# Optimization experiments

Measured on AMD Instinct MI355X. Metric: run time of the kernel, lower is better.

The kernel has to match this reference:

```python
import jax, jax.numpy as jnp
import numpy as np

NEG = 9000000000000000.0  # large negative multiplier from the original code

def setup_inputs() -> dict:
    key = jax.random.key(0)
    ks = jax.random.split(key, 7)
    B, N, DIN, H, DOUT = 128, 512, 256, 256, 256
    x = jax.random.normal(ks[0], (B, N, DIN), dtype=jnp.float32)
    # binary float mask (1 = attend, 0 = blocked), as used multiplicatively in the module
    mask = (jax.random.uniform(ks[1], (B, N, N)) > 0.5).astype(jnp.float32)
    def lin(k, fan_in, fan_out):
        kw, kb = jax.random.split(k)
        bound = 1.0 / np.sqrt(fan_in)
        W = jax.random.uniform(kw, (fan_in, fan_out), minval=-bound, maxval=bound, dtype=jnp.float32)
        b = jax.random.uniform(kb, (fan_out,), minval=-bound, maxval=bound, dtype=jnp.float32)
        return W, b
    Wv, bv = lin(ks[2], DIN, H)
    Wk, bk = lin(ks[3], DIN, H)
    Wq, bq = lin(ks[4], DIN, H)
    Wo, bo = lin(ks[5], H, DOUT)
    return {"x": x, "mask": mask, "Wv": Wv, "bv": bv, "Wk": Wk, "bk": bk,
            "Wq": Wq, "bq": bq, "Wo": Wo, "bo": bo}

def reference(x, mask, Wv, bv, Wk, bk, Wq, bq, Wo, bo):
    # x: [B,N,din], mask: [B,N,N]
    v = jax.nn.relu(jnp.einsum('bnd,dh->bnh', x, Wv) + bv)   # [B,N,H]
    q = jax.nn.relu(jnp.einsum('bnd,dh->bnh', x, Wq) + bq)   # [B,N,H]
    k = jax.nn.relu(jnp.einsum('bnd,dh->bnh', x, Wk) + bk)   # [B,N,H]
    scores = jnp.einsum('bnh,bmh->bnm', q, k)                 # [B,N,N]
    att = jax.nn.softmax(scores * mask - NEG * (1.0 - mask), axis=2)
    out = jnp.einsum('bnm,bmh->bnh', att, v)                  # [B,N,H]
    out = jax.nn.relu(jnp.einsum('bnh,ho->bno', out, Wo) + bo)
    return out
```

## Files before the change

### kernel.cpp

```cpp
#include <hip/hip_runtime.h>
#include <stdint.h>

typedef __attribute__((ext_vector_type(8))) __bf16 bf16x8;
typedef __attribute__((ext_vector_type(4))) float f32x4;
typedef __attribute__((ext_vector_type(8))) unsigned short ushort8;
typedef __attribute__((ext_vector_type(4))) unsigned short ushort4v;
typedef unsigned short u16;
typedef unsigned int u32;

__device__ __forceinline__ u16 f2bf(float f) {
    __bf16 h = (__bf16)f;
    return __builtin_bit_cast(u16, h);
}

__device__ __forceinline__ f32x4 mfma16(bf16x8 a, bf16x8 b, f32x4 c) {
    return __builtin_amdgcn_mfma_f32_16x16x32_bf16(a, b, c, 0, 0, 0);
}

typedef __attribute__((address_space(1))) const char g_char;
typedef __attribute__((address_space(3))) char l_char;
__device__ __forceinline__ void gload_lds16(const void* g, void* l) {
    __builtin_amdgcn_global_load_lds((g_char*)g, (l_char*)l, 16, 0, 0);
}

__global__ __launch_bounds__(256) void prep_w(
    const float* __restrict__ Wq, const float* __restrict__ Wk,
    const float* __restrict__ Wv, const float* __restrict__ Wo,
    u16* __restrict__ WT, u16* __restrict__ WOT)
{
    int idx = blockIdx.x * 256 + threadIdx.x;
    if (idx < 196608) {
        int j = idx >> 8, k = idx & 255;
        const float* W = (j < 256) ? Wq : (j < 512) ? Wk : Wv;
        WT[idx] = f2bf(W[k * 256 + (j & 255)]);
    } else {
        int t = idx - 196608;
        int j = t >> 8, k = t & 255;
        WOT[t] = f2bf(Wo[k * 256 + j]);
    }
}

__global__ __launch_bounds__(256, 2) void qkv_gemm(
    const float* __restrict__ X, const u16* __restrict__ WT,
    const float* __restrict__ bQ, const float* __restrict__ bK,
    const float* __restrict__ bV,
    u16* __restrict__ outQ, u16* __restrict__ outK, u16* __restrict__ outVT)
{
    __shared__ __align__(16) u16 As[128 * 256];
    __shared__ __align__(16) u16 Bs[128 * 64];
    const int tid = threadIdx.x;
    const int m0 = blockIdx.x * 128;

    #pragma unroll
    for (int i = 0; i < 32; ++i) {
        int flat = (i * 256 + tid) * 4;
        int r = flat >> 8, c = flat & 255;
        const f32x4 f = *reinterpret_cast<const f32x4*>(X + (size_t)(m0 + r) * 256 + c);
        ushort4v h;
        h.x = f2bf(f.x); h.y = f2bf(f.y); h.z = f2bf(f.z); h.w = f2bf(f.w);
        int byte = (r * 512 + c * 2) ^ ((r & 7) << 4);
        *reinterpret_cast<ushort4v*>(reinterpret_cast<char*>(As) + byte) = h;
    }

    const int lane = tid & 63, wid = tid >> 6;
    const int wr = wid >> 1, wc = wid & 1;
    const int lr = lane & 15, lg = lane >> 4;

    for (int cb = 0; cb < 6; ++cb) {
        const int jbase = cb * 128;
        f32x4 acc[4][4];
        #pragma unroll
        for (int a = 0; a < 4; ++a)
            #pragma unroll
            for (int b = 0; b < 4; ++b) acc[a][b] = (f32x4){0.f, 0.f, 0.f, 0.f};

        for (int kk = 0; kk < 256; kk += 64) {
            __syncthreads();
            #pragma unroll
            for (int i = 0; i < 4; ++i) {
                int e = (i * 256 + tid) * 8;
                int r = e >> 6, c = e & 63;
                ushort8 d = *reinterpret_cast<const ushort8*>(WT + (size_t)(jbase + r) * 256 + kk + c);
                int byte = (r * 128 + c * 2) ^ ((r & 7) << 4);
                *reinterpret_cast<ushort8*>(reinterpret_cast<char*>(Bs) + byte) = d;
            }
            __syncthreads();
            #pragma unroll
            for (int ks = 0; ks < 2; ++ks) {
                bf16x8 af[4], bfr[4];
                #pragma unroll
                for (int mt = 0; mt < 4; ++mt) {
                    int r = wr * 64 + mt * 16 + lr;
                    int byte = (r * 512 + (kk + ks * 32 + lg * 8) * 2) ^ ((r & 7) << 4);
                    af[mt] = *reinterpret_cast<const bf16x8*>(reinterpret_cast<const char*>(As) + byte);
                }
                #pragma unroll
                for (int nt = 0; nt < 4; ++nt) {
                    int r = wc * 64 + nt * 16 + lr;
                    int byte = (r * 128 + (ks * 32 + lg * 8) * 2) ^ ((r & 7) << 4);
                    bfr[nt] = *reinterpret_cast<const bf16x8*>(reinterpret_cast<const char*>(Bs) + byte);
                }
                #pragma unroll
                for (int mt = 0; mt < 4; ++mt)
                    #pragma unroll
                    for (int nt = 0; nt < 4; ++nt)
                        acc[mt][nt] = mfma16(af[mt], bfr[nt], acc[mt][nt]);
            }
        }
        const float* bias = (cb < 2) ? bQ : (cb < 4) ? bK : bV;
        float bcol[4];
        #pragma unroll
        for (int nt = 0; nt < 4; ++nt)
            bcol[nt] = bias[(jbase + wc * 64 + nt * 16 + lr) & 255];
        #pragma unroll
        for (int mt = 0; mt < 4; ++mt) {
            #pragma unroll
            for (int nt = 0; nt < 4; ++nt) {
                #pragma unroll
                for (int j = 0; j < 4; ++j) {
                    float v = fmaxf(acc[mt][nt][j] + bcol[nt], 0.f);
                    u16 h = f2bf(v);
                    int row = m0 + wr * 64 + mt * 16 + lg * 4 + j;
                    int col = jbase + wc * 64 + nt * 16 + lr;
                    if (cb < 2) {
                        outQ[(size_t)row * 256 + col] = h;
                    } else if (cb < 4) {
                        outK[(size_t)row * 256 + (col - 256)] = h;
                    } else {
                        int bb = row >> 9, n = row & 511;
                        outVT[(size_t)bb * 131072 + (size_t)(col - 512) * 512 + n] = h;
                    }
                }
            }
        }
    }
}

__global__ __launch_bounds__(512) void attn_kernel(
    const u16* __restrict__ Q, const u16* __restrict__ K,
    const u16* __restrict__ VT, const float* __restrict__ Mask,
    u16* __restrict__ Out)
{
    __shared__ __align__(16) u16 k_lds[2][32 * 256];
    __shared__ __align__(16) u16 v_lds[2][256 * 32];
    __shared__ __align__(16) char p_lds[8 * 1280];
    const int tid = threadIdx.x;
    const int b  = blockIdx.x & 127;
    const int rb = blockIdx.x >> 7;
    const int lane = tid & 63, wid = tid >> 6;
    const int lr = lane & 15, lg = lane >> 4;
    const int n0 = rb * 128 + wid * 16;
    const u16* qbat = Q  + (size_t)b * 131072;
    const u16* kbat = K  + (size_t)b * 131072;
    const u16* vbat = VT + (size_t)b * 131072;
    const float* mbase = Mask + ((size_t)b * 512 + n0 + lr) * 512;
    char* pw = p_lds + wid * 1280;

    auto stage = [&](int buf, int kt) {
        #pragma unroll
        for (int i = 0; i < 2; ++i) {
            int p = (i * 512 + tid) * 16;
            int krow = p >> 9, kcol2 = p & 511;
            int scol2 = kcol2 ^ ((krow & 7) << 4);
            const char* gk = reinterpret_cast<const char*>(kbat + (size_t)(kt * 32 + krow) * 256) + scol2;
            char* lk = reinterpret_cast<char*>(k_lds[buf]) + i * 8192 + wid * 1024;
            gload_lds16(gk, lk);
            int vrow = p >> 6;
            int chunk = (p >> 4) & 3;
            int schunk = chunk ^ (vrow & 3);
            const char* gv = reinterpret_cast<const char*>(vbat + (size_t)vrow * 512 + kt * 32) + schunk * 16;
            char* lv = reinterpret_cast<char*>(v_lds[buf]) + i * 8192 + wid * 1024;
            gload_lds16(gv, lv);
        }
    };

    bf16x8 qf[8];
    #pragma unroll
    for (int ks = 0; ks < 8; ++ks)
        qf[ks] = *reinterpret_cast<const bf16x8*>(
            qbat + (size_t)(n0 + lr) * 256 + ks * 32 + lg * 8);

    stage(0, 0);
    f32x4 mf[2];
    #pragma unroll
    for (int ct = 0; ct < 2; ++ct)
        mf[ct] = __builtin_nontemporal_load(
            reinterpret_cast<const f32x4*>(mbase + ct * 16 + lg * 4));

    f32x4 acc[16];
    #pragma unroll
    for (int i = 0; i < 16; ++i) acc[i] = (f32x4){0.f, 0.f, 0.f, 0.f};
    float mreg = -__builtin_inff(), lreg = 0.f;

    __syncthreads();

    for (int kt = 0; kt < 16; ++kt) {
        const int cur = kt & 1;
        if (kt < 15) stage(cur ^ 1, kt + 1);

        u32 mb = 0;
        #pragma unroll
        for (int ct = 0; ct < 2; ++ct)
            #pragma unroll
            for (int j = 0; j < 4; ++j)
                mb |= (mf[ct][j] > 0.5f ? 1u : 0u) << (ct * 4 + j);
        if (kt < 15) {
            #pragma unroll
            for (int ct = 0; ct < 2; ++ct)
                mf[ct] = __builtin_nontemporal_load(reinterpret_cast<const f32x4*>(
                    mbase + (kt + 1) * 32 + ct * 16 + lg * 4));
        }

        f32x4 s[2];
        s[0] = (f32x4){0.f, 0.f, 0.f, 0.f};
        s[1] = (f32x4){0.f, 0.f, 0.f, 0.f};
        const char* kbase = reinterpret_cast<const char*>(k_lds[cur]);
        __builtin_amdgcn_s_setprio(1);
        #pragma unroll
        for (int ks = 0; ks < 8; ++ks) {
            #pragma unroll
            for (int ct = 0; ct < 2; ++ct) {
                int krow = ct * 16 + lr;
                int byte = (krow * 512 + (ks * 32 + lg * 8) * 2) ^ ((krow & 7) << 4);
                bf16x8 kf = *reinterpret_cast<const bf16x8*>(kbase + byte);
                s[ct] = mfma16(kf, qf[ks], s[ct]);
            }
        }
        __builtin_amdgcn_s_setprio(0);

        float p[2][4];
        #pragma unroll
        for (int ct = 0; ct < 2; ++ct)
            #pragma unroll
            for (int j = 0; j < 4; ++j)
                p[ct][j] = ((mb >> (ct * 4 + j)) & 1u) ? s[ct][j] : -9.0e15f;

        float r0 = p[0][0];
        r0 = fmaxf(r0, p[0][1]); r0 = fmaxf(r0, p[0][2]); r0 = fmaxf(r0, p[0][3]);
        r0 = fmaxf(r0, p[1][0]); r0 = fmaxf(r0, p[1][1]);
        r0 = fmaxf(r0, p[1][2]); r0 = fmaxf(r0, p[1][3]);
        r0 = fmaxf(r0, __shfl_xor(r0, 16));
        r0 = fmaxf(r0, __shfl_xor(r0, 32));
        bool need = (r0 > mreg);
        if (__any(need)) {
            float mnew = fmaxf(mreg, r0);
            float sc = __expf(mreg - mnew);
            mreg = mnew;
            lreg *= sc;
            #pragma unroll
            for (int ht = 0; ht < 16; ++ht) {
                acc[ht][0] *= sc; acc[ht][1] *= sc;
                acc[ht][2] *= sc; acc[ht][3] *= sc;
            }
        }
        float ps = 0.f;
        #pragma unroll
        for (int ct = 0; ct < 2; ++ct)
            #pragma unroll
            for (int j = 0; j < 4; ++j) {
                float e = __expf(p[ct][j] - mreg);
                p[ct][j] = e;
                ps += e;
            }
        lreg += ps;

        #pragma unroll
        for (int ct = 0; ct < 2; ++ct) {
            ushort4v w;
            w.x = f2bf(p[ct][0]); w.y = f2bf(p[ct][1]);
            w.z = f2bf(p[ct][2]); w.w = f2bf(p[ct][3]);
            *reinterpret_cast<ushort4v*>(pw + lr * 80 + ct * 32 + lg * 8) = w;
        }

        bf16x8 pf = *reinterpret_cast<const bf16x8*>(pw + lr * 80 + lg * 16);
        const char* vbase = reinterpret_cast<const char*>(v_lds[cur]);
        __builtin_amdgcn_s_setprio(1);
        #pragma unroll
        for (int ht = 0; ht < 16; ++ht) {
            int hrow = ht * 16 + lr;
            int byte = (hrow * 64 + lg * 16) ^ ((hrow & 3) << 4);
            bf16x8 vf = *reinterpret_cast<const bf16x8*>(vbase + byte);
            acc[ht] = mfma16(vf, pf, acc[ht]);
        }
        __builtin_amdgcn_s_setprio(0);

        __syncthreads();
    }

    float lt = lreg;
    lt += __shfl_xor(lt, 16);
    lt += __shfl_xor(lt, 32);
    float inv = 1.0f / lt;
    u16* orow = Out + ((size_t)b * 512 + n0 + lr) * 256;
    #pragma unroll
    for (int ht = 0; ht < 16; ++ht) {
        ushort4v w;
        w.x = f2bf(acc[ht][0] * inv); w.y = f2bf(acc[ht][1] * inv);
        w.z = f2bf(acc[ht][2] * inv); w.w = f2bf(acc[ht][3] * inv);
        *reinterpret_cast<ushort4v*>(orow + ht * 16 + lg * 4) = w;
    }
}

__global__ __launch_bounds__(256, 2) void out_gemm(
    const u16* __restrict__ A, const u16* __restrict__ WOT,
    const float* __restrict__ bO, float* __restrict__ Out)
{
    __shared__ __align__(16) u16 As[128 * 256];
    __shared__ __align__(16) u16 Bs[128 * 64];
    const int tid = threadIdx.x;
    const int m0 = blockIdx.x * 128;

    #pragma unroll
    for (int i = 0; i < 16; ++i) {
        int e = (i * 256 + tid) * 8;
        int r = e >> 8, c = e & 255;
        ushort8 d = *reinterpret_cast<const ushort8*>(A + (size_t)(m0 + r) * 256 + c);
        int byte = (r * 512 + c * 2) ^ ((r & 7) << 4);
        *reinterpret_cast<ushort8*>(reinterpret_cast<char*>(As) + byte) = d;
    }

    const int lane = tid & 63, wid = tid >> 6;
    const int wr = wid >> 1, wc = wid & 1;
    const int lr = lane & 15, lg = lane >> 4;

    for (int cb = 0; cb < 2; ++cb) {
        const int jbase = cb * 128;
        f32x4 acc[4][4];
        #pragma unroll
        for (int a = 0; a < 4; ++a)
            #pragma unroll
            for (int b = 0; b < 4; ++b) acc[a][b] = (f32x4){0.f, 0.f, 0.f, 0.f};

        for (int kk = 0; kk < 256; kk += 64) {
            __syncthreads();
            #pragma unroll
            for (int i = 0; i < 4; ++i) {
                int e = (i * 256 + tid) * 8;
                int r = e >> 6, c = e & 63;
                ushort8 d = *reinterpret_cast<const ushort8*>(WOT + (size_t)(jbase + r) * 256 + kk + c);
                int byte = (r * 128 + c * 2) ^ ((r & 7) << 4);
                *reinterpret_cast<ushort8*>(reinterpret_cast<char*>(Bs) + byte) = d;
            }
            __syncthreads();
            #pragma unroll
            for (int ks = 0; ks < 2; ++ks) {
                bf16x8 af[4], bfr[4];
                #pragma unroll
                for (int mt = 0; mt < 4; ++mt) {
                    int r = wr * 64 + mt * 16 + lr;
                    int byte = (r * 512 + (kk + ks * 32 + lg * 8) * 2) ^ ((r & 7) << 4);
                    af[mt] = *reinterpret_cast<const bf16x8*>(reinterpret_cast<const char*>(As) + byte);
                }
                #pragma unroll
                for (int nt = 0; nt < 4; ++nt) {
                    int r = wc * 64 + nt * 16 + lr;
                    int byte = (r * 128 + (ks * 32 + lg * 8) * 2) ^ ((r & 7) << 4);
                    bfr[nt] = *reinterpret_cast<const bf16x8*>(reinterpret_cast<const char*>(Bs) + byte);
                }
                #pragma unroll
                for (int mt = 0; mt < 4; ++mt)
                    #pragma unroll
                    for (int nt = 0; nt < 4; ++nt)
                        acc[mt][nt] = mfma16(af[mt], bfr[nt], acc[mt][nt]);
            }
        }
        float bcol[4];
        #pragma unroll
        for (int nt = 0; nt < 4; ++nt)
            bcol[nt] = bO[jbase + wc * 64 + nt * 16 + lr];
        #pragma unroll
        for (int mt = 0; mt < 4; ++mt) {
            #pragma unroll
            for (int nt = 0; nt < 4; ++nt) {
                #pragma unroll
                for (int j = 0; j < 4; ++j) {
                    float v = fmaxf(acc[mt][nt][j] + bcol[nt], 0.f);
                    int row = m0 + wr * 64 + mt * 16 + lg * 4 + j;
                    int col = jbase + wc * 64 + nt * 16 + lr;
                    Out[(size_t)row * 256 + col] = v;
                }
            }
        }
    }
}

extern "C" void kernel_launch(void* const* d_in, const int* in_sizes, int n_in,
                              void* d_out, int out_size, void* d_ws, size_t ws_size,
                              hipStream_t stream) {
    const float* x    = (const float*)d_in[0];
    const float* mask = (const float*)d_in[1];
    const float* Wv   = (const float*)d_in[2];
    const float* bv   = (const float*)d_in[3];
    const float* Wk   = (const float*)d_in[4];
    const float* bk   = (const float*)d_in[5];
    const float* Wq   = (const float*)d_in[6];
    const float* bq   = (const float*)d_in[7];
    const float* Wo   = (const float*)d_in[8];
    const float* bo   = (const float*)d_in[9];
    float* out = (float*)d_out;

    char* ws = (char*)d_ws;
    u16* WT  = (u16*)(ws);
    u16* WOT = (u16*)(ws + 393216);
    u16* Qb  = (u16*)(ws + 524288);
    u16* Kb  = (u16*)(ws + 524288 + 33554432);
    u16* VTb = (u16*)(ws + 524288 + 2 * 33554432);

    prep_w<<<1024, 256, 0, stream>>>(Wq, Wk, Wv, Wo, WT, WOT);
    qkv_gemm<<<512, 256, 0, stream>>>(x, WT, bq, bk, bv, Qb, Kb, VTb);
    attn_kernel<<<512, 512, 0, stream>>>(Qb, Kb, VTb, mask, Qb);
    out_gemm<<<512, 256, 0, stream>>>(Qb, WOT, bo, out);
}
```

Before: 187.5 us.

## Split QKV GEMM per column block with double-buffered async weight staging

The QKV projection now launches one block per (row tile, 128-column block), 3072 blocks instead of 512. Each block streams X in 64-wide K slices through double-buffered LDS rather than holding the full 128x256 A tile. prep_w pre-swizzles the weights into K-sliced chunks so they can be copied straight to LDS with global_load_lds while the current slice computes, and MFMA sections get raised priority. The aim is more parallelism, smaller LDS use and overlap of loads with compute, at the cost of reading and converting X six times instead of once.

```diff
diff --git a/kernel.cpp b/kernel.cpp
--- a/kernel.cpp
+++ b/kernel.cpp
@@ -26,13 +26,15 @@
 __global__ __launch_bounds__(256) void prep_w(
     const float* __restrict__ Wq, const float* __restrict__ Wk,
     const float* __restrict__ Wv, const float* __restrict__ Wo,
-    u16* __restrict__ WT, u16* __restrict__ WOT)
+    u16* __restrict__ WTs, u16* __restrict__ WOT)
 {
     int idx = blockIdx.x * 256 + threadIdx.x;
     if (idx < 196608) {
         int j = idx >> 8, k = idx & 255;
         const float* W = (j < 256) ? Wq : (j < 512) ? Wk : Wv;
-        WT[idx] = f2bf(W[k * 256 + (j & 255)]);
+        u16 v = f2bf(W[k * 256 + (j & 255)]);
+        int kk = k >> 6, c = k & 63;
+        WTs[kk * 49152 + j * 64 + (c ^ ((j & 7) << 3))] = v;
     } else {
         int t = idx - 196608;
         int j = t >> 8, k = t & 255;
@@ -40,11 +42,300 @@
     }
 }
 
-__global__ __launch_bounds__(256, 2) void qkv_gemm(
-    const float* __restrict__ X, const u16* __restrict__ WT,
+__global__ __launch_bounds__(256) void qkv_gemm(
+    const float* __restrict__ X, const u16* __restrict__ WTs,
     const float* __restrict__ bQ, const float* __restrict__ bK,
     const float* __restrict__ bV,
     u16* __restrict__ outQ, u16* __restrict__ outK, u16* __restrict__ outVT)
+{
+    __shared__ __align__(16) u16 As[2][8192];
+    __shared__ __align__(16) u16 Bs[2][8192];
+    const int tid = threadIdx.x;
+    const int bid = blockIdx.x;
+    const int m0 = (bid / 6) * 128;
+    const int cbi = bid - (bid / 6) * 6;
+    const int jbase = cbi * 128;
+
+    const int lane = tid & 63, wid = tid >> 6;
+    const int wr = wid >> 1, wc = wid & 1;
+    const int lr = lane & 15, lg = lane >> 4;
+
+    auto stageB = [&](int buf, int kk) {
+        const char* src = reinterpret_cast<const char*>(
+            WTs + (size_t)kk * 49152 + (size_t)jbase * 64);
+        #pragma unroll
+        for (int i = 0; i < 4; ++i) {
+            int p = (i * 256 + tid) * 16;
+            gload_lds16(src + p,
+                reinterpret_cast<char*>(Bs[buf]) + i * 4096 + wid * 1024);
+        }
+    };
+
+    f32x4 ar[8];
+    auto issueA = [&](int kk) {
+        #pragma unroll
+        for (int i = 0; i < 8; ++i) {
+            int e = (i * 256 + tid) * 4;
+            int r = e >> 6, c = e & 63;
+            ar[i] = *reinterpret_cast<const f32x4*>(
+                X + (size_t)(m0 + r) * 256 + kk * 64 + c);
+        }
+    };
+    auto writeA = [&](int buf) {
+        #pragma unroll
+        for (int i = 0; i < 8; ++i) {
+            int e = (i * 256 + tid) * 4;
+            int r = e >> 6, c = e & 63;
+            ushort4v h;
+            h.x = f2bf(ar[i].x); h.y = f2bf(ar[i].y);
+            h.z = f2bf(ar[i].z); h.w = f2bf(ar[i].w);
+            int byte = (r * 128 + c * 2) ^ ((r & 7) << 4);
+            *reinterpret_cast<ushort4v*>(reinterpret_cast<char*>(As[buf]) + byte) = h;
+        }
+    };
+
+    f32x4 acc[4][4];
+    #pragma unroll
+    for (int a = 0; a < 4; ++a)
+        #pragma unroll
+        for (int b = 0; b < 4; ++b) acc[a][b] = (f32x4){0.f, 0.f, 0.f, 0.f};
+
+    stageB(0, 0);
+    issueA(0);
+    writeA(0);
+    __syncthreads();
+
+    for (int kk = 0; kk < 4; ++kk) {
+        const int cur = kk & 1;
+        if (kk < 3) {
+            stageB(cur ^ 1, kk + 1);
+            issueA(kk + 1);
+        }
+        #pragma unroll
+        for (int ks = 0; ks < 2; ++ks) {
+            bf16x8 af[4], bfr[4];
+            #pragma unroll
+            for (int mt = 0; mt < 4; ++mt) {
+                int r = wr * 64 + mt * 16 + lr;
+                int byte = (r * 128 + ks * 64 + lg * 16) ^ ((r & 7) << 4);
+                af[mt] = *reinterpret_cast<const bf16x8*>(
+                    reinterpret_cast<const char*>(As[cur]) + byte);
+            }
+            #pragma unroll
+            for (int nt = 0; nt < 4; ++nt) {
+                int r = wc * 64 + nt * 16 + lr;
+                int byte = (r * 128 + ks * 64 + lg * 16) ^ ((r & 7) << 4);
+                bfr[nt] = *reinterpret_cast<const bf16x8*>(
+                    reinterpret_cast<const char*>(Bs[cur]) + byte);
+            }
+            __builtin_amdgcn_s_setprio(1);
+            #pragma unroll
+            for (int mt = 0; mt < 4; ++mt)
+                #pragma unroll
+                for (int nt = 0; nt < 4; ++nt)
+                    acc[mt][nt] = mfma16(af[mt], bfr[nt], acc[mt][nt]);
+            __builtin_amdgcn_s_setprio(0);
+        }
+        if (kk < 3) writeA(cur ^ 1);
+        __syncthreads();
+    }
+
+    const float* bias = (cbi < 2) ? bQ : (cbi < 4) ? bK : bV;
+    float bcol[4];
+    #pragma unroll
+    for (int nt = 0; nt < 4; ++nt)
+        bcol[nt] = bias[(jbase + wc * 64 + nt * 16 + lr) & 255];
+    #pragma unroll
+    for (int mt = 0; mt < 4; ++mt) {
+        #pragma unroll
+        for (int nt = 0; nt < 4; ++nt) {
+            #pragma unroll
+            for (int j = 0; j < 4; ++j) {
+                float v = fmaxf(acc[mt][nt][j] + bcol[nt], 0.f);
+                u16 h = f2bf(v);
+                int row = m0 + wr * 64 + mt * 16 + lg * 4 + j;
+                int col = jbase + wc * 64 + nt * 16 + lr;
+                if (cbi < 2) {
+                    outQ[(size_t)row * 256 + col] = h;
+                } else if (cbi < 4) {
+                    outK[(size_t)row * 256 + (col - 256)] = h;
+                } else {
+                    int bb = row >> 9, n = row & 511;
+                    outVT[(size_t)bb * 131072 + (size_t)(col - 512) * 512 + n] = h;
+                }
+            }
+        }
+    }
+}
+
+__global__ __launch_bounds__(512) void attn_kernel(
+    const u16* __restrict__ Q, const u16* __restrict__ K,
+    const u16* __restrict__ VT, const float* __restrict__ Mask,
+    u16* __restrict__ Out)
+{
+    __shared__ __align__(16) u16 k_lds[2][32 * 256];
+    __shared__ __align__(16) u16 v_lds[2][256 * 32];
+    __shared__ __align__(16) char p_lds[8 * 1280];
+    const int tid = threadIdx.x;
+    const int b  = blockIdx.x & 127;
+    const int rb = blockIdx.x >> 7;
+    const int lane = tid & 63, wid = tid >> 6;
+    const int lr = lane & 15, lg = lane >> 4;
+    const int n0 = rb * 128 + wid * 16;
+    const u16* qbat = Q  + (size_t)b * 131072;
+    const u16* kbat = K  + (size_t)b * 131072;
+    const u16* vbat = VT + (size_t)b * 131072;
+    const float* mbase = Mask + ((size_t)b * 512 + n0 + lr) * 512;
+    char* pw = p_lds + wid * 1280;
+
+    auto stage = [&](int buf, int kt) {
+        #pragma unroll
+        for (int i = 0; i < 2; ++i) {
+            int p = (i * 512 + tid) * 16;
+            int krow = p >> 9, kcol2 = p & 511;
+            int scol2 = kcol2 ^ ((krow & 7) << 4);
+            const char* gk = reinterpret_cast<const char*>(kbat + (size_t)(kt * 32 + krow) * 256) + scol2;
+            char* lk = reinterpret_cast<char*>(k_lds[buf]) + i * 8192 + wid * 1024;
+            gload_lds16(gk, lk);
+            int vrow = p >> 6;
+            int chunk = (p >> 4) & 3;
+            int schunk = chunk ^ (vrow & 3);
+            const char* gv = reinterpret_cast<const char*>(vbat + (size_t)vrow * 512 + kt * 32) + schunk * 16;
+            char* lv = reinterpret_cast<char*>(v_lds[buf]) + i * 8192 + wid * 1024;
+            gload_lds16(gv, lv);
+        }
+    };
+
+    bf16x8 qf[8];
+    #pragma unroll
+    for (int ks = 0; ks < 8; ++ks)
+        qf[ks] = *reinterpret_cast<const bf16x8*>(
+            qbat + (size_t)(n0 + lr) * 256 + ks * 32 + lg * 8);
+
+    stage(0, 0);
+    f32x4 mf[2];
+    #pragma unroll
+    for (int ct = 0; ct < 2; ++ct)
+        mf[ct] = __builtin_nontemporal_load(
+            reinterpret_cast<const f32x4*>(mbase + ct * 16 + lg * 4));
+
+    f32x4 acc[16];
+    #pragma unroll
+    for (int i = 0; i < 16; ++i) acc[i] = (f32x4){0.f, 0.f, 0.f, 0.f};
+    float mreg = -__builtin_inff(), lreg = 0.f;
+
+    __syncthreads();
+
+    for (int kt = 0; kt < 16; ++kt) {
+        const int cur = kt & 1;
+        if (kt < 15) stage(cur ^ 1, kt + 1);
+
+        u32 mb = 0;
+        #pragma unroll
+        for (int ct = 0; ct < 2; ++ct)
+            #pragma unroll
+            for (int j = 0; j < 4; ++j)
+                mb |= (mf[ct][j] > 0.5f ? 1u : 0u) << (ct * 4 + j);
+        if (kt < 15) {
+            #pragma unroll
+            for (int ct = 0; ct < 2; ++ct)
+                mf[ct] = __builtin_nontemporal_load(reinterpret_cast<const f32x4*>(
+                    mbase + (kt + 1) * 32 + ct * 16 + lg * 4));
+        }
+
+        f32x4 s[2];
+        s[0] = (f32x4){0.f, 0.f, 0.f, 0.f};
+        s[1] = (f32x4){0.f, 0.f, 0.f, 0.f};
+        const char* kbase = reinterpret_cast<const char*>(k_lds[cur]);
+        __builtin_amdgcn_s_setprio(1);
+        #pragma unroll
+        for (int ks = 0; ks < 8; ++ks) {
+            #pragma unroll
+            for (int ct = 0; ct < 2; ++ct) {
+                int krow = ct * 16 + lr;
+                int byte = (krow * 512 + (ks * 32 + lg * 8) * 2) ^ ((krow & 7) << 4);
+                bf16x8 kf = *reinterpret_cast<const bf16x8*>(kbase + byte);
+                s[ct] = mfma16(kf, qf[ks], s[ct]);
+            }
+        }
+        __builtin_amdgcn_s_setprio(0);
+
+        float p[2][4];
+        #pragma unroll
+        for (int ct = 0; ct < 2; ++ct)
+            #pragma unroll
+            for (int j = 0; j < 4; ++j)
+                p[ct][j] = ((mb >> (ct * 4 + j)) & 1u) ? s[ct][j] : -9.0e15f;
+
+        float r0 = p[0][0];
+        r0 = fmaxf(r0, p[0][1]); r0 = fmaxf(r0, p[0][2]); r0 = fmaxf(r0, p[0][3]);
+        r0 = fmaxf(r0, p[1][0]); r0 = fmaxf(r0, p[1][1]);
+        r0 = fmaxf(r0, p[1][2]); r0 = fmaxf(r0, p[1][3]);
+        r0 = fmaxf(r0, __shfl_xor(r0, 16));
+        r0 = fmaxf(r0, __shfl_xor(r0, 32));
+        bool need = (r0 > mreg);
+        if (__any(need)) {
+            float mnew = fmaxf(mreg, r0);
+            float sc = __expf(mreg - mnew);
+            mreg = mnew;
+            lreg *= sc;
+            #pragma unroll
+            for (int ht = 0; ht < 16; ++ht) {
+                acc[ht][0] *= sc; acc[ht][1] *= sc;
+                acc[ht][2] *= sc; acc[ht][3] *= sc;
+            }
+        }
+        float ps = 0.f;
+        #pragma unroll
+        for (int ct = 0; ct < 2; ++ct)
+            #pragma unroll
+            for (int j = 0; j < 4; ++j) {
+                float e = __expf(p[ct][j] - mreg);
+                p[ct][j] = e;
+                ps += e;
+            }
+        lreg += ps;
+
+        #pragma unroll
+        for (int ct = 0; ct < 2; ++ct) {
+            ushort4v w;
+            w.x = f2bf(p[ct][0]); w.y = f2bf(p[ct][1]);
+            w.z = f2bf(p[ct][2]); w.w = f2bf(p[ct][3]);
+            *reinterpret_cast<ushort4v*>(pw + lr * 80 + ct * 32 + lg * 8) = w;
+        }
+
+        bf16x8 pf = *reinterpret_cast<const bf16x8*>(pw + lr * 80 + lg * 16);
+        const char* vbase = reinterpret_cast<const char*>(v_lds[cur]);
+        __builtin_amdgcn_s_setprio(1);
+        #pragma unroll
+        for (int ht = 0; ht < 16; ++ht) {
+            int hrow = ht * 16 + lr;
+            int byte = (hrow * 64 + lg * 16) ^ ((hrow & 3) << 4);
+            bf16x8 vf = *reinterpret_cast<const bf16x8*>(vbase + byte);
+            acc[ht] = mfma16(vf, pf, acc[ht]);
+        }
+        __builtin_amdgcn_s_setprio(0);
+
+        __syncthreads();
+    }
+
+    float lt = lreg;
+    lt += __shfl_xor(lt, 16);
+    lt += __shfl_xor(lt, 32);
+    float inv = 1.0f / lt;
+    u16* orow = Out + ((size_t)b * 512 + n0 + lr) * 256;
+    #pragma unroll
+    for (int ht = 0; ht < 16; ++ht) {
+        ushort4v w;
+        w.x = f2bf(acc[ht][0] * inv); w.y = f2bf(acc[ht][1] * inv);
+        w.z = f2bf(acc[ht][2] * inv); w.w = f2bf(acc[ht][3] * inv);
+        *reinterpret_cast<ushort4v*>(orow + ht * 16 + lg * 4) = w;
+    }
+}
+
+__global__ __launch_bounds__(256, 2) void out_gemm(
+    const u16* __restrict__ A, const u16* __restrict__ WOT,
+    const float* __restrict__ bO, float* __restrict__ Out)
 {
     __shared__ __align__(16) u16 As[128 * 256];
     __shared__ __align__(16) u16 Bs[128 * 64];
@@ -52,21 +343,19 @@
     const int m0 = blockIdx.x * 128;
 
     #pragma unroll
-    for (int i = 0; i < 32; ++i) {
-        int flat = (i * 256 + tid) * 4;
-        int r = flat >> 8, c = flat & 255;
-        const f32x4 f = *reinterpret_cast<const f32x4*>(X + (size_t)(m0 + r) * 256 + c);
-        ushort4v h;
-        h.x = f2bf(f.x); h.y = f2bf(f.y); h.z = f2bf(f.z); h.w = f2bf(f.w);
+    for (int i = 0; i < 16; ++i) {
+        int e = (i * 256 + tid) * 8;
+        int r = e >> 8, c = e & 255;
+        ushort8 d = *reinterpret_cast<const ushort8*>(A + (size_t)(m0 + r) * 256 + c);
         int byte = (r * 512 + c * 2) ^ ((r & 7) << 4);
-        *reinterpret_cast<ushort4v*>(reinterpret_cast<char*>(As) + byte) = h;
+        *reinterpret_cast<ushort8*>(reinterpret_cast<char*>(As) + byte) = d;
     }
 
     const int lane = tid & 63, wid = tid >> 6;
     const int wr = wid >> 1, wc = wid & 1;
     const int lr = lane & 15, lg = lane >> 4;
 
-    for (int cb = 0; cb < 6; ++cb) {
+    for (int cb = 0; cb < 2; ++cb) {
         const int jbase = cb * 128;
         f32x4 acc[4][4];
         #pragma unroll
@@ -80,7 +369,7 @@
             for (int i = 0; i < 4; ++i) {
                 int e = (i * 256 + tid) * 8;
                 int r = e >> 6, c = e & 63;
-                ushort8 d = *reinterpret_cast<const ushort8*>(WT + (size_t)(jbase + r) * 256 + kk + c);
+                ushort8 d = *reinterpret_cast<const ushort8*>(WOT + (size_t)(jbase + r) * 256 + kk + c);
                 int byte = (r * 128 + c * 2) ^ ((r & 7) << 4);
                 *reinterpret_cast<ushort8*>(reinterpret_cast<char*>(Bs) + byte) = d;
             }
@@ -107,263 +396,6 @@
                         acc[mt][nt] = mfma16(af[mt], bfr[nt], acc[mt][nt]);
             }
         }
-        const float* bias = (cb < 2) ? bQ : (cb < 4) ? bK : bV;
-        float bcol[4];
-        #pragma unroll
-        for (int nt = 0; nt < 4; ++nt)
-            bcol[nt] = bias[(jbase + wc * 64 + nt * 16 + lr) & 255];
-        #pragma unroll
-        for (int mt = 0; mt < 4; ++mt) {
-            #pragma unroll
-            for (int nt = 0; nt < 4; ++nt) {
-                #pragma unroll
-                for (int j = 0; j < 4; ++j) {
-                    float v = fmaxf(acc[mt][nt][j] + bcol[nt], 0.f);
-                    u16 h = f2bf(v);
-                    int row = m0 + wr * 64 + mt * 16 + lg * 4 + j;
-                    int col = jbase + wc * 64 + nt * 16 + lr;
-                    if (cb < 2) {
-                        outQ[(size_t)row * 256 + col] = h;
-                    } else if (cb < 4) {
-                        outK[(size_t)row * 256 + (col - 256)] = h;
-                    } else {
-                        int bb = row >> 9, n = row & 511;
-                        outVT[(size_t)bb * 131072 + (size_t)(col - 512) * 512 + n] = h;
-                    }
-                }
-            }
-        }
-    }
-}
-
-__global__ __launch_bounds__(512) void attn_kernel(
-    const u16* __restrict__ Q, const u16* __restrict__ K,
-    const u16* __restrict__ VT, const float* __restrict__ Mask,
-    u16* __restrict__ Out)
-{
-    __shared__ __align__(16) u16 k_lds[2][32 * 256];
-    __shared__ __align__(16) u16 v_lds[2][256 * 32];
-    __shared__ __align__(16) char p_lds[8 * 1280];
-    const int tid = threadIdx.x;
-    const int b  = blockIdx.x & 127;
-    const int rb = blockIdx.x >> 7;
-    const int lane = tid & 63, wid = tid >> 6;
-    const int lr = lane & 15, lg = lane >> 4;
-    const int n0 = rb * 128 + wid * 16;
-    const u16* qbat = Q  + (size_t)b * 131072;
-    const u16* kbat = K  + (size_t)b * 131072;
-    const u16* vbat = VT + (size_t)b * 131072;
-    const float* mbase = Mask + ((size_t)b * 512 + n0 + lr) * 512;
-    char* pw = p_lds + wid * 1280;
-
-    auto stage = [&](int buf, int kt) {
-        #pragma unroll
-        for (int i = 0; i < 2; ++i) {
-            int p = (i * 512 + tid) * 16;
-            int krow = p >> 9, kcol2 = p & 511;
-            int scol2 = kcol2 ^ ((krow & 7) << 4);
-            const char* gk = reinterpret_cast<const char*>(kbat + (size_t)(kt * 32 + krow) * 256) + scol2;
-            char* lk = reinterpret_cast<char*>(k_lds[buf]) + i * 8192 + wid * 1024;
-            gload_lds16(gk, lk);
-            int vrow = p >> 6;
-            int chunk = (p >> 4) & 3;
-            int schunk = chunk ^ (vrow & 3);
-            const char* gv = reinterpret_cast<const char*>(vbat + (size_t)vrow * 512 + kt * 32) + schunk * 16;
-            char* lv = reinterpret_cast<char*>(v_lds[buf]) + i * 8192 + wid * 1024;
-            gload_lds16(gv, lv);
-        }
-    };
-
-    bf16x8 qf[8];
-    #pragma unroll
-    for (int ks = 0; ks < 8; ++ks)
-        qf[ks] = *reinterpret_cast<const bf16x8*>(
-            qbat + (size_t)(n0 + lr) * 256 + ks * 32 + lg * 8);
-
-    stage(0, 0);
-    f32x4 mf[2];
-    #pragma unroll
-    for (int ct = 0; ct < 2; ++ct)
-        mf[ct] = __builtin_nontemporal_load(
-            reinterpret_cast<const f32x4*>(mbase + ct * 16 + lg * 4));
-
-    f32x4 acc[16];
-    #pragma unroll
-    for (int i = 0; i < 16; ++i) acc[i] = (f32x4){0.f, 0.f, 0.f, 0.f};
-    float mreg = -__builtin_inff(), lreg = 0.f;
-
-    __syncthreads();
-
-    for (int kt = 0; kt < 16; ++kt) {
-        const int cur = kt & 1;
-        if (kt < 15) stage(cur ^ 1, kt + 1);
-
-        u32 mb = 0;
-        #pragma unroll
-        for (int ct = 0; ct < 2; ++ct)
-            #pragma unroll
-            for (int j = 0; j < 4; ++j)
-                mb |= (mf[ct][j] > 0.5f ? 1u : 0u) << (ct * 4 + j);
-        if (kt < 15) {
-            #pragma unroll
-            for (int ct = 0; ct < 2; ++ct)
-                mf[ct] = __builtin_nontemporal_load(reinterpret_cast<const f32x4*>(
-                    mbase + (kt + 1) * 32 + ct * 16 + lg * 4));
-        }
-
-        f32x4 s[2];
-        s[0] = (f32x4){0.f, 0.f, 0.f, 0.f};
-        s[1] = (f32x4){0.f, 0.f, 0.f, 0.f};
-        const char* kbase = reinterpret_cast<const char*>(k_lds[cur]);
-        __builtin_amdgcn_s_setprio(1);
-        #pragma unroll
-        for (int ks = 0; ks < 8; ++ks) {
-            #pragma unroll
-            for (int ct = 0; ct < 2; ++ct) {
-                int krow = ct * 16 + lr;
-                int byte = (krow * 512 + (ks * 32 + lg * 8) * 2) ^ ((krow & 7) << 4);
-                bf16x8 kf = *reinterpret_cast<const bf16x8*>(kbase + byte);
-                s[ct] = mfma16(kf, qf[ks], s[ct]);
-            }
-        }
-        __builtin_amdgcn_s_setprio(0);
-
-        float p[2][4];
-        #pragma unroll
-        for (int ct = 0; ct < 2; ++ct)
-            #pragma unroll
-            for (int j = 0; j < 4; ++j)
-                p[ct][j] = ((mb >> (ct * 4 + j)) & 1u) ? s[ct][j] : -9.0e15f;
-
-        float r0 = p[0][0];
-        r0 = fmaxf(r0, p[0][1]); r0 = fmaxf(r0, p[0][2]); r0 = fmaxf(r0, p[0][3]);
-        r0 = fmaxf(r0, p[1][0]); r0 = fmaxf(r0, p[1][1]);
-        r0 = fmaxf(r0, p[1][2]); r0 = fmaxf(r0, p[1][3]);
-        r0 = fmaxf(r0, __shfl_xor(r0, 16));
-        r0 = fmaxf(r0, __shfl_xor(r0, 32));
-        bool need = (r0 > mreg);
-        if (__any(need)) {
-            float mnew = fmaxf(mreg, r0);
-            float sc = __expf(mreg - mnew);
-            mreg = mnew;
-            lreg *= sc;
-            #pragma unroll
-            for (int ht = 0; ht < 16; ++ht) {
-                acc[ht][0] *= sc; acc[ht][1] *= sc;
-                acc[ht][2] *= sc; acc[ht][3] *= sc;
-            }
-        }
-        float ps = 0.f;
-        #pragma unroll
-        for (int ct = 0; ct < 2; ++ct)
-            #pragma unroll
-            for (int j = 0; j < 4; ++j) {
-                float e = __expf(p[ct][j] - mreg);
-                p[ct][j] = e;
-                ps += e;
-            }
-        lreg += ps;
-
-        #pragma unroll
-        for (int ct = 0; ct < 2; ++ct) {
-            ushort4v w;
-            w.x = f2bf(p[ct][0]); w.y = f2bf(p[ct][1]);
-            w.z = f2bf(p[ct][2]); w.w = f2bf(p[ct][3]);
-            *reinterpret_cast<ushort4v*>(pw + lr * 80 + ct * 32 + lg * 8) = w;
-        }
-
-        bf16x8 pf = *reinterpret_cast<const bf16x8*>(pw + lr * 80 + lg * 16);
-        const char* vbase = reinterpret_cast<const char*>(v_lds[cur]);
-        __builtin_amdgcn_s_setprio(1);
-        #pragma unroll
-        for (int ht = 0; ht < 16; ++ht) {
-            int hrow = ht * 16 + lr;
-            int byte = (hrow * 64 + lg * 16) ^ ((hrow & 3) << 4);
-            bf16x8 vf = *reinterpret_cast<const bf16x8*>(vbase + byte);
-            acc[ht] = mfma16(vf, pf, acc[ht]);
-        }
-        __builtin_amdgcn_s_setprio(0);
-
-        __syncthreads();
-    }
-
-    float lt = lreg;
-    lt += __shfl_xor(lt, 16);
-    lt += __shfl_xor(lt, 32);
-    float inv = 1.0f / lt;
-    u16* orow = Out + ((size_t)b * 512 + n0 + lr) * 256;
-    #pragma unroll
-    for (int ht = 0; ht < 16; ++ht) {
-        ushort4v w;
-        w.x = f2bf(acc[ht][0] * inv); w.y = f2bf(acc[ht][1] * inv);
-        w.z = f2bf(acc[ht][2] * inv); w.w = f2bf(acc[ht][3] * inv);
-        *reinterpret_cast<ushort4v*>(orow + ht * 16 + lg * 4) = w;
-    }
-}
-
-__global__ __launch_bounds__(256, 2) void out_gemm(
-    const u16* __restrict__ A, const u16* __restrict__ WOT,
-    const float* __restrict__ bO, float* __restrict__ Out)
-{
-    __shared__ __align__(16) u16 As[128 * 256];
-    __shared__ __align__(16) u16 Bs[128 * 64];
-    const int tid = threadIdx.x;
-    const int m0 = blockIdx.x * 128;
-
-    #pragma unroll
-    for (int i = 0; i < 16; ++i) {
-        int e = (i * 256 + tid) * 8;
-        int r = e >> 8, c = e & 255;
-        ushort8 d = *reinterpret_cast<const ushort8*>(A + (size_t)(m0 + r) * 256 + c);
-        int byte = (r * 512 + c * 2) ^ ((r & 7) << 4);
-        *reinterpret_cast<ushort8*>(reinterpret_cast<char*>(As) + byte) = d;
-    }
-
-    const int lane = tid & 63, wid = tid >> 6;
-    const int wr = wid >> 1, wc = wid & 1;
-    const int lr = lane & 15, lg = lane >> 4;
-
-    for (int cb = 0; cb < 2; ++cb) {
-        const int jbase = cb * 128;
-        f32x4 acc[4][4];
-        #pragma unroll
-        for (int a = 0; a < 4; ++a)
-            #pragma unroll
-            for (int b = 0; b < 4; ++b) acc[a][b] = (f32x4){0.f, 0.f, 0.f, 0.f};
-
-        for (int kk = 0; kk < 256; kk += 64) {
-            __syncthreads();
-            #pragma unroll
-            for (int i = 0; i < 4; ++i) {
-                int e = (i * 256 + tid) * 8;
-                int r = e >> 6, c = e & 63;
-                ushort8 d = *reinterpret_cast<const ushort8*>(WOT + (size_t)(jbase + r) * 256 + kk + c);
-                int byte = (r * 128 + c * 2) ^ ((r & 7) << 4);
-                *reinterpret_cast<ushort8*>(reinterpret_cast<char*>(Bs) + byte) = d;
-            }
-            __syncthreads();
-            #pragma unroll
-            for (int ks = 0; ks < 2; ++ks) {
-                bf16x8 af[4], bfr[4];
-                #pragma unroll
-                for (int mt = 0; mt < 4; ++mt) {
-                    int r = wr * 64 + mt * 16 + lr;
-                    int byte = (r * 512 + (kk + ks * 32 + lg * 8) * 2) ^ ((r & 7) << 4);
-                    af[mt] = *reinterpret_cast<const bf16x8*>(reinterpret_cast<const char*>(As) + byte);
-                }
-                #pragma unroll
-                for (int nt = 0; nt < 4; ++nt) {
-                    int r = wc * 64 + nt * 16 + lr;
-                    int byte = (r * 128 + (ks * 32 + lg * 8) * 2) ^ ((r & 7) << 4);
-                    bfr[nt] = *reinterpret_cast<const bf16x8*>(reinterpret_cast<const char*>(Bs) + byte);
-                }
-                #pragma unroll
-                for (int mt = 0; mt < 4; ++mt)
-                    #pragma unroll
-                    for (int nt = 0; nt < 4; ++nt)
-                        acc[mt][nt] = mfma16(af[mt], bfr[nt], acc[mt][nt]);
-            }
-        }
         float bcol[4];
         #pragma unroll
         for (int nt = 0; nt < 4; ++nt)
@@ -400,14 +432,14 @@
     float* out = (float*)d_out;
 
     char* ws = (char*)d_ws;
-    u16* WT  = (u16*)(ws);
+    u16* WTs = (u16*)(ws);
     u16* WOT = (u16*)(ws + 393216);
     u16* Qb  = (u16*)(ws + 524288);
     u16* Kb  = (u16*)(ws + 524288 + 33554432);
     u16* VTb = (u16*)(ws + 524288 + 2 * 33554432);
 
-    prep_w<<<1024, 256, 0, stream>>>(Wq, Wk, Wv, Wo, WT, WOT);
-    qkv_gemm<<<512, 256, 0, stream>>>(x, WT, bq, bk, bv, Qb, Kb, VTb);
+    prep_w<<<1024, 256, 0, stream>>>(Wq, Wk, Wv, Wo, WTs, WOT);
+    qkv_gemm<<<3072, 256, 0, stream>>>(x, WTs, bq, bk, bv, Qb, Kb, VTb);
     attn_kernel<<<512, 512, 0, stream>>>(Qb, Kb, VTb, mask, Qb);
     out_gemm<<<512, 256, 0, stream>>>(Qb, WOT, bo, out);
 }
```

New measurement: 212.3 us. 13.3% more time.

## Double-buffer QKV weight tiles via direct global-to-LDS loads with pre-swizzled layout

Applied to the files above, without the earlier changes.

The weight transpose kernel now writes W in a pre-swizzled, k-chunk-major layout so the QKV GEMM can stream B tiles straight into LDS with global_load_lds. The B tile is double-buffered and the next tile is prefetched while MFMAs run on the current one, removing one barrier per k step. MFMA sections get raised wave priority. LDS usage grows by one B buffer and the occupancy hint of 2 blocks per CU is dropped, which may reduce occupancy.

```diff
diff --git a/kernel.cpp b/kernel.cpp
--- a/kernel.cpp
+++ b/kernel.cpp
@@ -26,13 +26,15 @@
 __global__ __launch_bounds__(256) void prep_w(
     const float* __restrict__ Wq, const float* __restrict__ Wk,
     const float* __restrict__ Wv, const float* __restrict__ Wo,
-    u16* __restrict__ WT, u16* __restrict__ WOT)
+    u16* __restrict__ WTs, u16* __restrict__ WOT)
 {
     int idx = blockIdx.x * 256 + threadIdx.x;
     if (idx < 196608) {
         int j = idx >> 8, k = idx & 255;
         const float* W = (j < 256) ? Wq : (j < 512) ? Wk : Wv;
-        WT[idx] = f2bf(W[k * 256 + (j & 255)]);
+        u16 v = f2bf(W[k * 256 + (j & 255)]);
+        int kk = k >> 6, c = k & 63;
+        WTs[kk * 49152 + j * 64 + (c ^ ((j & 7) << 3))] = v;
     } else {
         int t = idx - 196608;
         int j = t >> 8, k = t & 255;
@@ -40,14 +42,14 @@
     }
 }
 
-__global__ __launch_bounds__(256, 2) void qkv_gemm(
-    const float* __restrict__ X, const u16* __restrict__ WT,
+__global__ __launch_bounds__(256) void qkv_gemm(
+    const float* __restrict__ X, const u16* __restrict__ WTs,
     const float* __restrict__ bQ, const float* __restrict__ bK,
     const float* __restrict__ bV,
     u16* __restrict__ outQ, u16* __restrict__ outK, u16* __restrict__ outVT)
 {
     __shared__ __align__(16) u16 As[128 * 256];
-    __shared__ __align__(16) u16 Bs[128 * 64];
+    __shared__ __align__(16) u16 Bs[2][8192];
     const int tid = threadIdx.x;
     const int m0 = blockIdx.x * 128;
 
@@ -66,6 +68,20 @@
     const int wr = wid >> 1, wc = wid & 1;
     const int lr = lane & 15, lg = lane >> 4;
 
+    auto stageB = [&](int buf, int cb, int kk) {
+        const char* src = reinterpret_cast<const char*>(
+            WTs + (size_t)kk * 49152 + (size_t)cb * 128 * 64);
+        #pragma unroll
+        for (int i = 0; i < 4; ++i) {
+            int p = (i * 256 + tid) * 16;
+            gload_lds16(src + p,
+                reinterpret_cast<char*>(Bs[buf]) + i * 4096 + wid * 1024);
+        }
+    };
+
+    stageB(0, 0, 0);
+    __syncthreads();
+
     for (int cb = 0; cb < 6; ++cb) {
         const int jbase = cb * 128;
         f32x4 acc[4][4];
@@ -74,39 +90,41 @@
             #pragma unroll
             for (int b = 0; b < 4; ++b) acc[a][b] = (f32x4){0.f, 0.f, 0.f, 0.f};
 
-        for (int kk = 0; kk < 256; kk += 64) {
-            __syncthreads();
-            #pragma unroll
-            for (int i = 0; i < 4; ++i) {
-                int e = (i * 256 + tid) * 8;
-                int r = e >> 6, c = e & 63;
-                ushort8 d = *reinterpret_cast<const ushort8*>(WT + (size_t)(jbase + r) * 256 + kk + c);
-                int byte = (r * 128 + c * 2) ^ ((r & 7) << 4);
-                *reinterpret_cast<ushort8*>(reinterpret_cast<char*>(Bs) + byte) = d;
-            }
-            __syncthreads();
+        for (int kk = 0; kk < 4; ++kk) {
+            const int t = cb * 4 + kk;
+            const int cur = t & 1;
+            if (t < 23) {
+                const int nt_ = t + 1;
+                stageB(cur ^ 1, nt_ >> 2, nt_ & 3);
+            }
             #pragma unroll
             for (int ks = 0; ks < 2; ++ks) {
                 bf16x8 af[4], bfr[4];
                 #pragma unroll
                 for (int mt = 0; mt < 4; ++mt) {
                     int r = wr * 64 + mt * 16 + lr;
-                    int byte = (r * 512 + (kk + ks * 32 + lg * 8) * 2) ^ ((r & 7) << 4);
-                    af[mt] = *reinterpret_cast<const bf16x8*>(reinterpret_cast<const char*>(As) + byte);
+                    int byte = (r * 512 + (kk * 64 + ks * 32 + lg * 8) * 2) ^ ((r & 7) << 4);
+                    af[mt] = *reinterpret_cast<const bf16x8*>(
+                        reinterpret_cast<const char*>(As) + byte);
                 }
                 #pragma unroll
                 for (int nt = 0; nt < 4; ++nt) {
                     int r = wc * 64 + nt * 16 + lr;
-                    int byte = (r * 128 + (ks * 32 + lg * 8) * 2) ^ ((r & 7) << 4);
-                    bfr[nt] = *reinterpret_cast<const bf16x8*>(reinterpret_cast<const char*>(Bs) + byte);
-                }
+                    int byte = (r * 128 + ks * 64 + lg * 16) ^ ((r & 7) << 4);
+                    bfr[nt] = *reinterpret_cast<const bf16x8*>(
+                        reinterpret_cast<const char*>(Bs[cur]) + byte);
+                }
+                __builtin_amdgcn_s_setprio(1);
                 #pragma unroll
                 for (int mt = 0; mt < 4; ++mt)
                     #pragma unroll
                     for (int nt = 0; nt < 4; ++nt)
                         acc[mt][nt] = mfma16(af[mt], bfr[nt], acc[mt][nt]);
-            }
-        }
+                __builtin_amdgcn_s_setprio(0);
+            }
+            __syncthreads();
+        }
+
         const float* bias = (cb < 2) ? bQ : (cb < 4) ? bK : bV;
         float bcol[4];
         #pragma unroll
@@ -400,14 +418,14 @@
     float* out = (float*)d_out;
 
     char* ws = (char*)d_ws;
-    u16* WT  = (u16*)(ws);
+    u16* WTs = (u16*)(ws);
     u16* WOT = (u16*)(ws + 393216);
     u16* Qb  = (u16*)(ws + 524288);
     u16* Kb  = (u16*)(ws + 524288 + 33554432);
     u16* VTb = (u16*)(ws + 524288 + 2 * 33554432);
 
-    prep_w<<<1024, 256, 0, stream>>>(Wq, Wk, Wv, Wo, WT, WOT);
-    qkv_gemm<<<512, 256, 0, stream>>>(x, WT, bq, bk, bv, Qb, Kb, VTb);
+    prep_w<<<1024, 256, 0, stream>>>(Wq, Wk, Wv, Wo, WTs, WOT);
+    qkv_gemm<<<512, 256, 0, stream>>>(x, WTs, bq, bk, bv, Qb, Kb, VTb);
     attn_kernel<<<512, 512, 0, stream>>>(Qb, Kb, VTb, mask, Qb);
     out_gemm<<<512, 256, 0, stream>>>(Qb, WOT, bo, out);
 }
```

New measurement: 208.0 us. 1.11x slower.
